# Kernel tuning notes

Hardware: AMD Instinct MI355X
Metric: run time of the kernel (lower is better)

Reference implementation:

```python
import math
import jax, jax.numpy as jnp
import numpy as np

B, SEQ, N_EMBD, N_HEAD, MAX_LEN = 2, 2048, 1024, 16, 2048
D_HEAD = N_EMBD // N_HEAD


def setup_inputs() -> dict:
    key = jax.random.key(0)
    k0, k1, k2, k3, k4 = jax.random.split(key, 5)
    x = jax.random.normal(k0, (B, SEQ, N_EMBD), jnp.float32)
    # nn.Linear weights stored [out_features, in_features]; scale ~ kaiming-ish
    s = 1.0 / math.sqrt(N_EMBD)
    Wq = jax.random.normal(k1, (N_EMBD, N_EMBD), jnp.float32) * s
    Wk = jax.random.normal(k2, (N_EMBD, N_EMBD), jnp.float32) * s
    Wv = jax.random.normal(k3, (N_EMBD, N_EMBD), jnp.float32) * s
    Er = jax.random.normal(k4, (MAX_LEN, D_HEAD), jnp.float32)
    return {"x": x, "Wq": Wq, "Wk": Wk, "Wv": Wv, "Er": Er}


def _skew(QEr):
    # QEr: [B, H, S, S]; mask with anti-diagonal tril-flip, then pad/reshape skew
    S = QEr.shape[-1]
    anti = jnp.flip(jnp.tril(jnp.ones((S, S), QEr.dtype)), axis=1)
    QEr = QEr * anti  # masked_fill(mask==0, 0)
    padded = jnp.pad(QEr, ((0, 0), (0, 0), (0, 0), (1, 0)))  # [B,H,S,S+1]
    Bq, H, S_, Sp1 = padded.shape
    return padded.reshape(Bq, H, Sp1, S_)[:, :, 1:, :]  # [B,H,S,S]


def reference(x, Wq, Wk, Wv, Er):
    Bx, S, E = x.shape
    H, d = N_HEAD, D_HEAD

    def proj(W):
        return jnp.einsum('bse,fe->bsf', x, W).reshape(Bx, S, H, d).transpose(0, 2, 1, 3)

    q, k, v = proj(Wq), proj(Wk), proj(Wv)  # [B,H,S,d]
    qk = jnp.einsum('bhqd,bhkd->bhqk', q, k)
    Er_s = Er[MAX_LEN - S:, :]  # [S, d]
    QEr = jnp.einsum('bhqd,rd->bhqr', q, Er_s)  # [B,H,S,S]
    Srel = _skew(QEr)
    attn = (qk + Srel) / math.sqrt(d)
    causal = jnp.tril(jnp.ones((S, S), bool))
    attn = jnp.where(causal, attn, -jnp.inf)
    p = jax.nn.softmax(attn, axis=-1)
    out = jnp.einsum('bhqk,bhkd->bhqd', p, v)
    return out.transpose(0, 2, 1, 3).reshape(Bx, S, E)
```

## Files before the change

kernel.cpp:

```cpp
#include <hip/hip_runtime.h>
#include <hip/hip_bf16.h>
#include <stdint.h>

#define S_LEN 2048
#define EMB   1024
#define NH    16
#define DH    64
#define BATCH 2

typedef short bf16x8 __attribute__((ext_vector_type(8)));
typedef short bf16x4 __attribute__((ext_vector_type(4)));
typedef float f32x4  __attribute__((ext_vector_type(4)));

__device__ __forceinline__ unsigned short f2bf(float f) {
    union { float f; unsigned int u; } v; v.f = f;
    unsigned int r = v.u + 0x7FFFu + ((v.u >> 16) & 1u);
    return (unsigned short)(r >> 16);
}

__device__ __forceinline__ short f2bf_fast(float f) {
    __hip_bfloat16 h = __float2bfloat16(f);
    return *reinterpret_cast<short*>(&h);
}

__device__ __forceinline__ bf16x8 load8f_to_bf(const float* __restrict__ p) {
    const float4* p4 = (const float4*)p;
    float4 x0 = p4[0];
    float4 x1 = p4[1];
    bf16x8 r;
    r[0] = (short)f2bf(x0.x); r[1] = (short)f2bf(x0.y);
    r[2] = (short)f2bf(x0.z); r[3] = (short)f2bf(x0.w);
    r[4] = (short)f2bf(x1.x); r[5] = (short)f2bf(x1.y);
    r[6] = (short)f2bf(x1.z); r[7] = (short)f2bf(x1.w);
    return r;
}

__device__ __forceinline__ void bar_lds() {
    asm volatile("s_waitcnt lgkmcnt(0)" ::: "memory");
    __builtin_amdgcn_sched_barrier(0);
    __builtin_amdgcn_s_barrier();
    __builtin_amdgcn_sched_barrier(0);
}

__device__ __forceinline__ void gload_lds16(const unsigned short* g, unsigned short* l) {
    __builtin_amdgcn_global_load_lds(
        (const __attribute__((address_space(1))) unsigned int*)g,
        (__attribute__((address_space(3))) unsigned int*)l, 16, 0, 0);
}

__global__ __launch_bounds__(256) void cvt_bf16(
    const float* __restrict__ x,  const float* __restrict__ wq,
    const float* __restrict__ wk, const float* __restrict__ wv,
    const float* __restrict__ er,
    unsigned short* __restrict__ xb, unsigned short* __restrict__ wb,
    unsigned short* __restrict__ erb)
{
    const int NX = 4194304 / 8, NW = 1048576 / 8, NE = 131072 / 8;
    const int total = NX + 3 * NW + NE;
    for (int i8 = blockIdx.x * 256 + threadIdx.x; i8 < total; i8 += gridDim.x * 256) {
        const float* src; unsigned short* dst; int off;
        if      (i8 < NX)          { src = x;  dst = xb;            off = i8; }
        else if (i8 < NX + NW)     { src = wq; dst = wb;            off = i8 - NX; }
        else if (i8 < NX + 2 * NW) { src = wk; dst = wb + 1048576;  off = i8 - NX - NW; }
        else if (i8 < NX + 3 * NW) { src = wv; dst = wb + 2097152;  off = i8 - NX - 2 * NW; }
        else                       { src = er; dst = erb;           off = i8 - NX - 3 * NW; }
        ((bf16x8*)dst)[off] = load8f_to_bf(src + (size_t)off * 8);
    }
}

__global__ __launch_bounds__(256) void proj_kernel_bf(
    const unsigned short* __restrict__ xb, const unsigned short* __restrict__ wb,
    unsigned short* __restrict__ Qb, unsigned short* __restrict__ Kb,
    unsigned short* __restrict__ Vt)
{
    __shared__ __align__(16) unsigned short Al[128 * 64];
    __shared__ __align__(16) unsigned short Bl[128 * 64];

    const int tid  = threadIdx.x;
    const int lane = tid & 63;
    const int w    = tid >> 6;
    const int wr   = w >> 1;
    const int wc   = w & 1;
    const int m0   = blockIdx.x * 128;
    const int c0   = blockIdx.y * 128;
    const int wsel = c0 >> 10;
    const int f0   = c0 & 1023;
    const unsigned short* __restrict__ W = wb + (size_t)wsel * 1048576;

    const int lr = lane & 15;
    const int g  = lane >> 4;

    const int srow8 = tid >> 3;
    const int scol  = (((tid & 7) ^ (srow8 & 7))) * 8;

    f32x4 acc[4][4];
#pragma unroll
    for (int i = 0; i < 4; i++)
#pragma unroll
        for (int n = 0; n < 4; n++) acc[i][n] = (f32x4){0.f, 0.f, 0.f, 0.f};

    for (int k0 = 0; k0 < 1024; k0 += 64) {
        __syncthreads();
#pragma unroll
        for (int i = 0; i < 4; i++) {
            gload_lds16(&xb[(size_t)(m0 + i * 32 + srow8) * 1024 + k0 + scol],
                        &Al[(i * 4 + w) * 512]);
            gload_lds16(&W [(size_t)(f0 + i * 32 + srow8) * 1024 + k0 + scol],
                        &Bl[(i * 4 + w) * 512]);
        }
        __syncthreads();

#pragma unroll
        for (int kk = 0; kk < 2; kk++) {
            bf16x8 a[4], b[4];
#pragma unroll
            for (int i = 0; i < 4; i++) {
                int ar = wr * 64 + i * 16 + lr;
                a[i] = *(const bf16x8*)&Al[ar * 64 + (((kk * 4 + g) ^ (ar & 7)) * 8)];
            }
#pragma unroll
            for (int n = 0; n < 4; n++) {
                int br = wc * 64 + n * 16 + lr;
                b[n] = *(const bf16x8*)&Bl[br * 64 + (((kk * 4 + g) ^ (br & 7)) * 8)];
            }
#pragma unroll
            for (int i = 0; i < 4; i++)
#pragma unroll
                for (int n = 0; n < 4; n++)
                    acc[i][n] = __builtin_amdgcn_mfma_f32_16x16x32_bf16(a[i], b[n], acc[i][n], 0, 0, 0);
        }
    }

#pragma unroll
    for (int i = 0; i < 4; i++) {
#pragma unroll
        for (int n = 0; n < 4; n++) {
#pragma unroll
            for (int j = 0; j < 4; j++) {
                int row_m = m0 + wr * 64 + i * 16 + g * 4 + j;
                int c     = c0 + wc * 64 + n * 16 + lr;
                int f     = c & 1023;
                int h     = f >> 6;
                int dd    = f & 63;
                int bb    = row_m >> 11;
                int s     = row_m & 2047;
                int bh    = bb * 16 + h;
                unsigned short bv = f2bf(acc[i][n][j]);
                if (wsel == 0)      Qb[((size_t)bh * 2048 + s) * 64 + dd] = bv;
                else if (wsel == 1) Kb[((size_t)bh * 2048 + s) * 64 + dd] = bv;
                else                Vt[((size_t)bh * 64 + dd) * 2048 + s] = bv;
            }
        }
    }
}

__global__ __launch_bounds__(256) void proj_kernel_f32(
    const float* __restrict__ x,
    const float* __restrict__ Wq, const float* __restrict__ Wk,
    const float* __restrict__ Wv,
    unsigned short* __restrict__ Qb, unsigned short* __restrict__ Kb,
    unsigned short* __restrict__ Vt)
{
    const int tid  = threadIdx.x;
    const int lane = tid & 63;
    const int w    = tid >> 6;
    const int wr   = w >> 1;
    const int wc   = w & 1;
    const int m0   = blockIdx.x * 128 + wr * 64;
    const int c0   = blockIdx.y * 128 + wc * 64;
    const int wsel = c0 >> 10;
    const int f0   = c0 & 1023;
    const float* __restrict__ W = (wsel == 0) ? Wq : (wsel == 1) ? Wk : Wv;

    const int lr = lane & 15;
    const int lk = (lane >> 4) * 8;

    f32x4 acc[4][4];
#pragma unroll
    for (int i = 0; i < 4; i++)
#pragma unroll
        for (int n = 0; n < 4; n++) acc[i][n] = (f32x4){0.f, 0.f, 0.f, 0.f};

    for (int k0 = 0; k0 < 1024; k0 += 32) {
        bf16x8 a[4], b[4];
#pragma unroll
        for (int i = 0; i < 4; i++)
            a[i] = load8f_to_bf(&x[(size_t)(m0 + i * 16 + lr) * 1024 + k0 + lk]);
#pragma unroll
        for (int n = 0; n < 4; n++)
            b[n] = load8f_to_bf(&W[(size_t)(f0 + n * 16 + lr) * 1024 + k0 + lk]);
#pragma unroll
        for (int i = 0; i < 4; i++)
#pragma unroll
            for (int n = 0; n < 4; n++)
                acc[i][n] = __builtin_amdgcn_mfma_f32_16x16x32_bf16(a[i], b[n], acc[i][n], 0, 0, 0);
    }

    const int g = lane >> 4;
#pragma unroll
    for (int i = 0; i < 4; i++) {
#pragma unroll
        for (int n = 0; n < 4; n++) {
#pragma unroll
            for (int j = 0; j < 4; j++) {
                int row_m = m0 + i * 16 + g * 4 + j;
                int c     = c0 + n * 16 + lr;
                int f     = c & 1023;
                int h     = f >> 6;
                int dd    = f & 63;
                int bb    = row_m >> 11;
                int s     = row_m & 2047;
                int bh    = bb * 16 + h;
                unsigned short bv = f2bf(acc[i][n][j]);
                if (wsel == 0)      Qb[((size_t)bh * 2048 + s) * 64 + dd] = bv;
                else if (wsel == 1) Kb[((size_t)bh * 2048 + s) * 64 + dd] = bv;
                else                Vt[((size_t)bh * 64 + dd) * 2048 + s] = bv;
            }
        }
    }
}

__global__ void cvt_er(const float* __restrict__ Er, unsigned short* __restrict__ Erb, int n)
{
    int i = blockIdx.x * 256 + threadIdx.x;
    if (i < n) Erb[i] = f2bf(Er[i]);
}

__global__ __launch_bounds__(256) void attn_kernel(
    const unsigned short* __restrict__ Qb, const unsigned short* __restrict__ Kb,
    const unsigned short* __restrict__ Vt, const unsigned short* __restrict__ Erb,
    float* __restrict__ out)
{
    __shared__ __align__(16) unsigned short Kl[64 * 64];
    __shared__ __align__(16) unsigned short Vl[64 * 64];
    __shared__ __align__(16) unsigned short El[128 * 64];
    __shared__ __align__(16) float          Rt[4][80][18];

    const int tid  = threadIdx.x;
    const int lane = tid & 63;
    const int w    = tid >> 6;

    const int i0  = blockIdx.x;
    const int xcd = i0 & 7;
    const int b2  = (i0 >> 3) & 3;
    const int qt  = 31 - (i0 >> 5);
    const int bh  = (xcd << 2) | b2;

    const int lr = lane & 15;
    const int g  = lane >> 4;
    const int lk = g * 8;

    const unsigned short* __restrict__ Qrow = Qb + (size_t)bh * 2048 * 64;
    const unsigned short* __restrict__ Krow = Kb + (size_t)bh * 2048 * 64;
    const unsigned short* __restrict__ Vrow = Vt + (size_t)bh * 64 * 2048;

    const float SCL = 0.125f * 1.44269504089f;
    const int bb  = bh >> 4;
    const int h   = bh & 15;
    const int q0  = qt * 64;
    const int q0w = q0 + w * 16;
    const int eoff = 48 - 16 * w;
    const int rbT0 = 1984 - q0;

    bf16x8 aq[2];
#pragma unroll
    for (int kk = 0; kk < 2; kk++)
        aq[kk] = *(const bf16x8*)&Qrow[(size_t)(q0w + lr) * 64 + kk * 32 + lk];

    f32x4 o[4];
#pragma unroll
    for (int m = 0; m < 4; m++) o[m] = (f32x4){0.f, 0.f, 0.f, 0.f};
    float mrow = -1e30f, lsum = 0.f;

    bf16x8 sk[2], sv[2], se[4];
    const int o8u = (tid & 7) * 8;

    auto kv_load = [&](int kt) {
        const int k0 = kt * 64;
#pragma unroll
        for (int i = 0; i < 2; i++) {
            int kr = ((i * 256 + tid) >> 3);
            sk[i] = *(const bf16x8*)&Krow[(size_t)(k0 + kr) * 64 + o8u];
        }
#pragma unroll
        for (int i = 0; i < 2; i++) {
            int d = ((i * 256 + tid) >> 3);
            sv[i] = *(const bf16x8*)&Vrow[(size_t)d * 2048 + k0 + o8u];
        }
    };
    auto kv_write = [&]() {
#pragma unroll
        for (int i = 0; i < 2; i++) {
            int kr = ((i * 256 + tid) >> 3);
            *(bf16x8*)&Kl[(kr * 64 + o8u) ^ ((kr & 7) << 3)] = sk[i];
        }
#pragma unroll
        for (int i = 0; i < 2; i++) {
            int d = ((i * 256 + tid) >> 3);
            *(bf16x8*)&Vl[(d * 64 + o8u) ^ ((d & 7) << 3)] = sv[i];
        }
    };
    auto e_load4 = [&](int base) {
#pragma unroll
        for (int i = 0; i < 4; i++) {
            int r = base + ((i * 256 + tid) >> 3);
            int rr = r > 2047 ? 2047 : r;
            se[i] = *(const bf16x8*)&Erb[(size_t)rr * 64 + o8u];
        }
    };
    auto e_load2 = [&](int base) {
#pragma unroll
        for (int i = 0; i < 2; i++) {
            int r = base + ((i * 256 + tid) >> 3);
            int rr = r > 2047 ? 2047 : r;
            se[i] = *(const bf16x8*)&Erb[(size_t)rr * 64 + o8u];
        }
    };
    auto e_write4 = [&](int base) {
#pragma unroll
        for (int i = 0; i < 4; i++) {
            int r = base + ((i * 256 + tid) >> 3);
            int slot = r & 127;
            *(bf16x8*)&El[(slot * 64 + o8u) ^ ((slot & 7) << 3)] = se[i];
        }
    };
    auto e_write2 = [&](int base) {
#pragma unroll
        for (int i = 0; i < 2; i++) {
            int r = base + ((i * 256 + tid) >> 3);
            int slot = r & 127;
            *(bf16x8*)&El[(slot * 64 + o8u) ^ ((slot & 7) << 3)] = se[i];
        }
    };

    kv_load(0);
    e_load4(rbT0);

#pragma unroll 1
    for (int kt = 0; kt <= qt; ++kt) {
        const int k0 = kt * 64;
        const int ep = ((qt ^ kt ^ 1) & 1) << 6;

        bar_lds();
        kv_write();
        if (kt == 0) e_write4(rbT0);
        else         e_write2(rbT0 + 64 * kt + 64);
        if (kt < qt) {
            kv_load(kt + 1);
            e_load2(rbT0 + 64 * kt + 128);
        }
        bar_lds();

        f32x4 s[4], r[5];
#pragma unroll
        for (int n = 0; n < 4; n++) s[n] = (f32x4){0.f, 0.f, 0.f, 0.f};
#pragma unroll
        for (int n = 0; n < 5; n++) r[n] = (f32x4){0.f, 0.f, 0.f, 0.f};
        __builtin_amdgcn_s_setprio(1);
#pragma unroll
        for (int kk = 0; kk < 2; kk++) {
            bf16x8 kb[4], be[5];
#pragma unroll
            for (int n = 0; n < 4; n++) {
                int kr = n * 16 + lr;
                kb[n] = *(const bf16x8*)&Kl[(kr * 64 + kk * 32 + lk) ^ ((kr & 7) << 3)];
            }
#pragma unroll
            for (int n = 0; n < 5; n++) {
                int er = (eoff + n * 16 + lr + ep) & 127;
                be[n] = *(const bf16x8*)&El[(er * 64 + kk * 32 + lk) ^ ((er & 7) << 3)];
            }
#pragma unroll
            for (int n = 0; n < 4; n++)
                s[n] = __builtin_amdgcn_mfma_f32_16x16x32_bf16(kb[n], aq[kk], s[n], 0, 0, 0);
#pragma unroll
            for (int n = 0; n < 5; n++)
                r[n] = __builtin_amdgcn_mfma_f32_16x16x32_bf16(be[n], aq[kk], r[n], 0, 0, 0);
        }
        __builtin_amdgcn_s_setprio(0);

#pragma unroll
        for (int n = 0; n < 5; n++)
#pragma unroll
            for (int j = 0; j < 4; j++)
                Rt[w][n * 16 + g * 4 + j][lr] = r[n][j];

        bar_lds();

        float pmax = -1e30f;
        if (kt != qt) {
#pragma unroll
            for (int n = 0; n < 4; n++)
#pragma unroll
                for (int j = 0; j < 4; j++) {
                    int wd = n * 16 + g * 4 + j + 15 - lr;
                    float sc = (s[n][j] + Rt[w][wd][lr]) * SCL;
                    s[n][j] = sc;
                    pmax = fmaxf(pmax, sc);
                }
        } else {
#pragma unroll
            for (int n = 0; n < 4; n++)
#pragma unroll
                for (int j = 0; j < 4; j++) {
                    int kl = n * 16 + g * 4 + j;
                    int wd = kl + 15 - lr;
                    float sc = (s[n][j] + Rt[w][wd][lr]) * SCL;
                    if (kl > w * 16 + lr) sc = -1e30f;
                    s[n][j] = sc;
                    pmax = fmaxf(pmax, sc);
                }
        }

        if (__any(pmax > mrow + 4.0f)) {
            pmax = fmaxf(pmax, __shfl_xor(pmax, 16));
            pmax = fmaxf(pmax, __shfl_xor(pmax, 32));
            float mn   = fmaxf(mrow, pmax);
            float corr = exp2f(mrow - mn);
            mrow = mn;
            lsum *= corr;
#pragma unroll
            for (int j = 0; j < 4; j++) {
                float cj = __shfl(corr, g * 4 + j);
#pragma unroll
                for (int m = 0; m < 4; m++) o[m][j] *= cj;
            }
        }

        float rs = 0.f;
        bf16x4 pa[4];
#pragma unroll
        for (int n = 0; n < 4; n++)
#pragma unroll
            for (int j = 0; j < 4; j++) {
                float pv = exp2f(s[n][j] - mrow);
                rs += pv;
                pa[n][j] = f2bf_fast(pv);
            }
        lsum += rs;

        __builtin_amdgcn_s_setprio(1);
#pragma unroll
        for (int m = 0; m < 4; m++) {
#pragma unroll
            for (int n = 0; n < 4; n++) {
                int d = 16 * m + lr;
                bf16x4 vb = *(const bf16x4*)&Vl[(d * 64 + 16 * n + 4 * g) ^ ((d & 7) << 3)];
                o[m] = __builtin_amdgcn_mfma_f32_16x16x16bf16_1k(pa[n], vb, o[m], 0, 0, 0);
            }
        }
        __builtin_amdgcn_s_setprio(0);
    }

    float ls = lsum;
    ls += __shfl_xor(ls, 16);
    ls += __shfl_xor(ls, 32);
    float linv = 1.0f / ls;
#pragma unroll
    for (int j = 0; j < 4; j++) {
        float lj = __shfl(linv, g * 4 + j);
#pragma unroll
        for (int m = 0; m < 4; m++) {
            int row = q0w + g * 4 + j;
            int col = h * 64 + 16 * m + lr;
            out[((size_t)bb * 2048 + row) * 1024 + col] = o[m][j] * lj;
        }
    }
}

extern "C" void kernel_launch(void* const* d_in, const int* in_sizes, int n_in,
                              void* d_out, int out_size, void* d_ws, size_t ws_size,
                              hipStream_t stream)
{
    const float* x  = (const float*)d_in[0];
    const float* Wq = (const float*)d_in[1];
    const float* Wk = (const float*)d_in[2];
    const float* Wv = (const float*)d_in[3];
    const float* Er = (const float*)d_in[4];
    float* out = (float*)d_out;

    char* ws = (char*)d_ws;
    const size_t MB = 1024 * 1024;
    unsigned short* Qb  = (unsigned short*)(ws);
    unsigned short* Kb  = (unsigned short*)(ws + 8  * MB);
    unsigned short* Vt  = (unsigned short*)(ws + 16 * MB);
    unsigned short* Erb = (unsigned short*)(ws + 24 * MB);
    unsigned short* xb  = (unsigned short*)(ws + 25 * MB);
    unsigned short* wb  = (unsigned short*)(ws + 33 * MB);

    if (ws_size >= (size_t)39 * MB) {
        cvt_bf16<<<dim3(1024), dim3(256), 0, stream>>>(x, Wq, Wk, Wv, Er, xb, wb, Erb);
        proj_kernel_bf<<<dim3(32, 24), dim3(256), 0, stream>>>(xb, wb, Qb, Kb, Vt);
    } else {
        cvt_er<<<dim3(512), dim3(256), 0, stream>>>(Er, Erb, 2048 * 64);
        proj_kernel_f32<<<dim3(32, 24), dim3(256), 0, stream>>>(x, Wq, Wk, Wv, Qb, Kb, Vt);
    }
    attn_kernel<<<dim3(1024), dim3(256), 0, stream>>>(Qb, Kb, Vt, Erb, out);
}
```

Measured before the change: 130.3 us.

## Load V directly from global into registers and prescale Q by softmax scale

V tiles are no longer staged through shared memory. Each wave now loads its own V fragments straight from global memory into registers at the start of each key tile, which removes the Vl LDS buffer and its writes and reads. Separately, Q is multiplied by the softmax scale once when it is loaded, so the per-score multiply in the inner loop goes away. The trade-off is that each of the 4 waves re-reads the same V tile from global or L2 with 8-byte loads. That adds redundant memory traffic and load latency in front of the first barrier, and rounding the prescaled Q to bf16 slightly changes precision.

```diff
diff --git a/kernel.cpp b/kernel.cpp
--- a/kernel.cpp
+++ b/kernel.cpp
@@ -21,6 +21,12 @@
 __device__ __forceinline__ short f2bf_fast(float f) {
     __hip_bfloat16 h = __float2bfloat16(f);
     return *reinterpret_cast<short*>(&h);
+}
+
+__device__ __forceinline__ float bf2f(short s) {
+    union { unsigned int u; float f; } v;
+    v.u = ((unsigned int)(unsigned short)s) << 16;
+    return v.f;
 }
 
 __device__ __forceinline__ bf16x8 load8f_to_bf(const float* __restrict__ p) {
@@ -232,7 +238,6 @@
     float* __restrict__ out)
 {
     __shared__ __align__(16) unsigned short Kl[64 * 64];
-    __shared__ __align__(16) unsigned short Vl[64 * 64];
     __shared__ __align__(16) unsigned short El[128 * 64];
     __shared__ __align__(16) float          Rt[4][80][18];
 
@@ -264,40 +269,35 @@
 
     bf16x8 aq[2];
 #pragma unroll
-    for (int kk = 0; kk < 2; kk++)
-        aq[kk] = *(const bf16x8*)&Qrow[(size_t)(q0w + lr) * 64 + kk * 32 + lk];
+    for (int kk = 0; kk < 2; kk++) {
+        bf16x8 q = *(const bf16x8*)&Qrow[(size_t)(q0w + lr) * 64 + kk * 32 + lk];
+#pragma unroll
+        for (int e = 0; e < 8; e++)
+            q[e] = f2bf_fast(bf2f(q[e]) * SCL);
+        aq[kk] = q;
+    }
 
     f32x4 o[4];
 #pragma unroll
     for (int m = 0; m < 4; m++) o[m] = (f32x4){0.f, 0.f, 0.f, 0.f};
     float mrow = -1e30f, lsum = 0.f;
 
-    bf16x8 sk[2], sv[2], se[4];
+    bf16x8 sk[2], se[4];
     const int o8u = (tid & 7) * 8;
 
-    auto kv_load = [&](int kt) {
+    auto k_load = [&](int kt) {
         const int k0 = kt * 64;
 #pragma unroll
         for (int i = 0; i < 2; i++) {
             int kr = ((i * 256 + tid) >> 3);
             sk[i] = *(const bf16x8*)&Krow[(size_t)(k0 + kr) * 64 + o8u];
         }
-#pragma unroll
-        for (int i = 0; i < 2; i++) {
-            int d = ((i * 256 + tid) >> 3);
-            sv[i] = *(const bf16x8*)&Vrow[(size_t)d * 2048 + k0 + o8u];
-        }
     };
-    auto kv_write = [&]() {
+    auto k_write = [&]() {
 #pragma unroll
         for (int i = 0; i < 2; i++) {
             int kr = ((i * 256 + tid) >> 3);
             *(bf16x8*)&Kl[(kr * 64 + o8u) ^ ((kr & 7) << 3)] = sk[i];
-        }
-#pragma unroll
-        for (int i = 0; i < 2; i++) {
-            int d = ((i * 256 + tid) >> 3);
-            *(bf16x8*)&Vl[(d * 64 + o8u) ^ ((d & 7) << 3)] = sv[i];
         }
     };
     auto e_load4 = [&](int base) {
@@ -333,7 +333,7 @@
         }
     };
 
-    kv_load(0);
+    k_load(0);
     e_load4(rbT0);
 
 #pragma unroll 1
@@ -341,12 +341,19 @@
         const int k0 = kt * 64;
         const int ep = ((qt ^ kt ^ 1) & 1) << 6;
 
+        bf16x4 vb[4][4];
+#pragma unroll
+        for (int m = 0; m < 4; m++)
+#pragma unroll
+            for (int n = 0; n < 4; n++)
+                vb[m][n] = *(const bf16x4*)&Vrow[(size_t)(16 * m + lr) * 2048 + k0 + 16 * n + 4 * g];
+
         bar_lds();
-        kv_write();
+        k_write();
         if (kt == 0) e_write4(rbT0);
         else         e_write2(rbT0 + 64 * kt + 64);
         if (kt < qt) {
-            kv_load(kt + 1);
+            k_load(kt + 1);
             e_load2(rbT0 + 64 * kt + 128);
         }
         bar_lds();
@@ -394,7 +401,7 @@
 #pragma unroll
                 for (int j = 0; j < 4; j++) {
                     int wd = n * 16 + g * 4 + j + 15 - lr;
-                    float sc = (s[n][j] + Rt[w][wd][lr]) * SCL;
+                    float sc = s[n][j] + Rt[w][wd][lr];
                     s[n][j] = sc;
                     pmax = fmaxf(pmax, sc);
                 }
@@ -405,7 +412,7 @@
                 for (int j = 0; j < 4; j++) {
                     int kl = n * 16 + g * 4 + j;
                     int wd = kl + 15 - lr;
-                    float sc = (s[n][j] + Rt[w][wd][lr]) * SCL;
+                    float sc = s[n][j] + Rt[w][wd][lr];
                     if (kl > w * 16 + lr) sc = -1e30f;
                     s[n][j] = sc;
                     pmax = fmaxf(pmax, sc);
@@ -441,14 +448,10 @@
 
         __builtin_amdgcn_s_setprio(1);
 #pragma unroll
-        for (int m = 0; m < 4; m++) {
-#pragma unroll
-            for (int n = 0; n < 4; n++) {
-                int d = 16 * m + lr;
-                bf16x4 vb = *(const bf16x4*)&Vl[(d * 64 + 16 * n + 4 * g) ^ ((d & 7) << 3)];
-                o[m] = __builtin_amdgcn_mfma_f32_16x16x16bf16_1k(pa[n], vb, o[m], 0, 0, 0);
-            }
-        }
+        for (int m = 0; m < 4; m++)
+#pragma unroll
+            for (int n = 0; n < 4; n++)
+                o[m] = __builtin_amdgcn_mfma_f32_16x16x16bf16_1k(pa[n], vb[m][n], o[m], 0, 0, 0);
         __builtin_amdgcn_s_setprio(0);
     }
 
```

Result: slower. 196.6 us (+50.9%).
